# Optimization experiments

Measured on AMD Instinct MI355X. Metric: run time of the kernel, lower is better.

## Reference

```python
import jax, jax.numpy as jnp
import numpy as np

B, T, H, W, C = 2, 6, 16, 16, 256
NUM_HEADS = 8


def light_cone_mask(T, H, W):
    """Boolean mask [N, N] (N = T*H*W): key (t,h,w) is visible to query
    (tq,hq,wq) iff t <= tq and |h-hq|, |w-wq| <= radius(tq, t), where
    radius = int(1 + (max(H,W)-1) * (tq-t) / max(tq,1))  (per the torch loop)."""
    M = max(H, W)
    tq = jnp.arange(T)[:, None]
    tk = jnp.arange(T)[None, :]
    # values are >= 0 on the causal region, so floor == int() truncation
    r = jnp.floor(1.0 + (M - 1) * (tq - tk) / jnp.maximum(tq, 1)).astype(jnp.int32)  # [T,T]
    causal = tk <= tq  # [T,T]
    dh = jnp.abs(jnp.arange(H)[:, None] - jnp.arange(H)[None, :])  # [Hq,Hk]
    dw = jnp.abs(jnp.arange(W)[:, None] - jnp.arange(W)[None, :])  # [Wq,Wk]
    m = (causal[:, None, None, :, None, None]
         & (dh[None, :, None, None, :, None] <= r[:, None, None, :, None, None])
         & (dw[None, None, :, None, None, :] <= r[:, None, None, :, None, None]))
    return m.reshape(T * H * W, T * H * W)


def setup_inputs() -> dict:
    key = jax.random.key(0)
    k1, k2, k3 = jax.random.split(key, 3)
    x = jax.random.normal(k1, (B, T, H, W, C), dtype=jnp.float32)
    Wqkv = jax.random.normal(k2, (C, 3 * C), dtype=jnp.float32) * 0.02
    Wo = jax.random.normal(k3, (C, C), dtype=jnp.float32) * 0.02
    bo = jnp.zeros((C,), dtype=jnp.float32)
    return {"x": x, "Wqkv": Wqkv, "Wo": Wo, "bo": bo}


def reference(x, Wqkv, Wo, bo):
    Bx, Tx, Hx, Wx, Cx = x.shape
    nh = NUM_HEADS
    hd = Cx // nh
    scale = hd ** (-0.5)
    N = Tx * Hx * Wx
    xt = x.reshape(Bx, N, Cx)
    qkv = (xt @ Wqkv).reshape(Bx, N, 3, nh, hd)
    q = qkv[:, :, 0].transpose(0, 2, 1, 3)  # [B, nh, N, hd]
    k = qkv[:, :, 1].transpose(0, 2, 1, 3)
    v = qkv[:, :, 2].transpose(0, 2, 1, 3)
    scores = jnp.einsum("bhqd,bhkd->bhqk", q, k) * scale  # [B, nh, N, N]
    mask = light_cone_mask(Tx, Hx, Wx)  # [N, N]
    neg = jnp.asarray(-1e9, dtype=scores.dtype)
    scores = jnp.where(mask[None, None, :, :], scores, neg)
    attn = jax.nn.softmax(scores, axis=-1)
    out = jnp.einsum("bhqk,bhkd->bhqd", attn, v)  # [B, nh, N, hd]
    out = out.transpose(0, 2, 1, 3).reshape(Bx, N, Cx)
    out = out @ Wo + bo
    return out.reshape(Bx, Tx, Hx, Wx, Cx)
```

## Files before the change

kernel.cpp:

```cpp
#include <hip/hip_runtime.h>
#include <hip/hip_bf16.h>

#define BB   2
#define TT   6
#define HH   16
#define WW   16
#define CC   256
#define NH   8
#define HD   32
#define NN   (TT*HH*WW)
#define BN   (BB*NN)
#define SCALE 0.17677669529663687f

typedef __attribute__((ext_vector_type(8))) short bf16x8;
typedef __attribute__((ext_vector_type(4))) short bf16x4;
typedef __attribute__((ext_vector_type(4))) float f32x4;
typedef __attribute__((ext_vector_type(16))) float f32x16;

static __device__ inline short f2b(float x) {
    __hip_bfloat16 h = __float2bfloat16(x);
    return __builtin_bit_cast(short, h);
}

__global__ __launch_bounds__(256) void gemm1_qkv(const float* __restrict__ x,
                                                 const float* __restrict__ Wqkv,
                                                 short* __restrict__ Qb,
                                                 short* __restrict__ Kb,
                                                 short* __restrict__ VT) {
    const int w = threadIdx.x >> 6, lane = threadIdx.x & 63;
    const int g = lane >> 4, c16 = lane & 15;
    const int ct = blockIdx.x % 12;
    const int rg = blockIdx.x / 12;
    const int n0 = ct * 64;
    const int mw = rg * 64 + w * 16;
    f32x4 acc[4] = {};
    #pragma unroll
    for (int ks = 0; ks < 8; ++ks) {
        const int k0 = ks * 32;
        const float* ap = x + (size_t)(mw + c16) * 256 + k0 + 8 * g;
        const float4 fa = *(const float4*)ap;
        const float4 fb = *(const float4*)(ap + 4);
        short ta[8] = { f2b(fa.x), f2b(fa.y), f2b(fa.z), f2b(fa.w),
                        f2b(fb.x), f2b(fb.y), f2b(fb.z), f2b(fb.w) };
        const bf16x8 a0 = *(bf16x8*)ta;
        #pragma unroll
        for (int ni = 0; ni < 4; ++ni) {
            const float* wp = Wqkv + (size_t)(k0 + 8 * g) * 768 + n0 + ni * 16 + c16;
            short tw[8];
            #pragma unroll
            for (int i = 0; i < 8; ++i) tw[i] = f2b(wp[(size_t)i * 768]);
            const bf16x8 bfr = *(bf16x8*)tw;
            acc[ni] = __builtin_amdgcn_mfma_f32_16x16x32_bf16(a0, bfr, acc[ni], 0, 0, 0);
        }
    }
    const int sec = ct >> 2;
    const int b = mw >= NN;
    const int nbase = mw - b * NN;
    #pragma unroll
    for (int ni = 0; ni < 4; ++ni) {
        const int col = n0 + ni * 16;
        const int h  = (col >> 5) & 7;
        const int d0 = col & 31;
        const int bh = b * 8 + h;
        if (sec == 2) {
            short t4[4];
            #pragma unroll
            for (int r = 0; r < 4; ++r) t4[r] = f2b(acc[ni][r]);
            const int kt  = nbase >> 5;
            const int klo = (nbase & 16) + 4 * g;
            size_t off = ((size_t)((bh * 48 + kt) * 32) + d0 + c16) * 32 + klo;
            *(bf16x4*)(VT + off) = *(bf16x4*)t4;
        } else {
            short* dst = (sec == 0) ? Qb : Kb;
            const float sc = (sec == 0) ? SCALE : 1.f;
            #pragma unroll
            for (int r = 0; r < 4; ++r)
                dst[((size_t)bh * NN + nbase + 4 * g + r) * 32 + d0 + c16] =
                    f2b(acc[ni][r] * sc);
        }
    }
}

__global__ __launch_bounds__(256) void attn_mfma32(const short* __restrict__ Qb,
                                                   const short* __restrict__ Kb,
                                                   const short* __restrict__ VT,
                                                   const float* __restrict__ Wo,
                                                   short* __restrict__ woT,
                                                   short* __restrict__ aob) {
    const int w    = threadIdx.x >> 6;
    const int lane = threadIdx.x & 63;
    const int l31  = lane & 31;
    const int gb   = lane >> 5;
    const int wq   = lane & 15;
    const int qh   = (lane >> 4) & 1;
    const int task = blockIdx.x;
    const int qt = task % 48, bh = task / 48;
    const int tqp = qt >> 4, hq = qt & 15;
    const int tq_a = 2 * tqp, tq_b = tq_a + 1;

    if (blockIdx.x < 32) {
        const int idx = blockIdx.x * 256 + threadIdx.x;
        const int k0 = (idx & 31) * 8;
        const int n  = idx >> 5;
        short t[8];
        #pragma unroll
        for (int j = 0; j < 8; ++j) t[j] = f2b(Wo[(size_t)(k0 + j) * 256 + n]);
        *(bf16x8*)(woT + (size_t)n * 256 + k0) = *(bf16x8*)t;
    }

    __shared__ int desc[64];
    __shared__ float sm_l[4][64];
    __shared__ float sm_acc[4][64][17];

    const int tq_l = qh ? tq_b : tq_a;
    const int qn   = tq_l * 256 + hq * 16 + wq;
    const short* QBH = Qb + (size_t)bh * NN * 32;
    const bf16x8 qf0 = *(const bf16x8*)(QBH + (size_t)qn * 32 + 8 * gb);
    const bf16x8 qf1 = *(const bf16x8*)(QBH + (size_t)qn * 32 + 16 + 8 * gb);

    int dwv[8];
    #pragma unroll
    for (int i = 0; i < 8; ++i) {
        int kl = (i & 3) + 8 * (i >> 2) + 4 * gb;
        int d = kl - wq; dwv[i] = d < 0 ? -d : d;
    }

    const int tqm_a = tq_a ? tq_a : 1;
    int ntiles = 0;
    int cst[6], h20[6], rtav[6], rtbv[6];
    #pragma unroll
    for (int tk = 0; tk < 6; ++tk) {
        int rb = 1 + (15 * (tq_b - tk)) / tq_b;
        int ra = (tk <= tq_a) ? (1 + (15 * (tq_a - tk)) / tqm_a) : -1;
        int lo = hq - rb; lo = lo < 0 ? 0 : lo;
        int hi = hq + rb; hi = hi > 15 ? 15 : hi;
        int c  = (tk <= tq_b) ? ((hi >> 1) - (lo >> 1) + 1) : 0;
        cst[tk] = ntiles; h20[tk] = lo >> 1; rtav[tk] = ra; rtbv[tk] = rb;
        ntiles += c;
    }

    if (w == 0) {
        const int t = lane;
        int dsc = 255;
        if (t < ntiles) {
            int sel = 0;
            #pragma unroll
            for (int tk = 1; tk < 6; ++tk)
                if (tk <= tq_b && t >= cst[tk]) sel = tk;
            const int hk2 = h20[sel] + (t - cst[sel]);
            dsc = ((sel * 256 + hk2 * 32) << 16) | ((rtav[sel] & 255) << 8) | (rtbv[sel] & 255);
        }
        desc[t] = dsc;
    }
    __syncthreads();

    const short* KBH = Kb + (size_t)bh * NN * 32;
    const short* VBH = VT + (size_t)bh * 48 * 32 * 32;

    f32x16 acc, zf16;
    #pragma unroll
    for (int r = 0; r < 16; ++r) { acc[r] = 0.f; zf16[r] = 0.f; }
    float l_run = 0.f;

    int pi = w;
    int dc = 0;
    bf16x8 kf0c = {}, kf1c = {}, vf0c = {}, vf1c = {};
    if (pi < ntiles) {
        dc = desc[pi];
        const int kb = dc >> 16;
        kf0c = *(const bf16x8*)(KBH + (size_t)(kb + l31) * 32 + 8 * gb);
        kf1c = *(const bf16x8*)(KBH + (size_t)(kb + l31) * 32 + 16 + 8 * gb);
        vf0c = *(const bf16x8*)(VBH + (size_t)((kb >> 5) * 32 + l31) * 32 + 8 * gb);
        vf1c = *(const bf16x8*)(VBH + (size_t)((kb >> 5) * 32 + l31) * 32 + 16 + 8 * gb);
    }
    while (pi < ntiles) {
        const int pn = pi + 4;
        const int pc = pn < ntiles ? pn : pi;
        const int dn = desc[pc];
        const int kbn = dn >> 16;
        const bf16x8 kf0n = *(const bf16x8*)(KBH + (size_t)(kbn + l31) * 32 + 8 * gb);
        const bf16x8 kf1n = *(const bf16x8*)(KBH + (size_t)(kbn + l31) * 32 + 16 + 8 * gb);
        const bf16x8 vf0n = *(const bf16x8*)(VBH + (size_t)((kbn >> 5) * 32 + l31) * 32 + 8 * gb);
        const bf16x8 vf1n = *(const bf16x8*)(VBH + (size_t)((kbn >> 5) * 32 + l31) * 32 + 16 + 8 * gb);

        const int rta = (dc << 16) >> 24;
        const int rtb = (dc << 24) >> 24;
        const int rt_l = qh ? rtb : rta;
        const int hk2 = (dc >> 21) & 7;
        const int t0 = 2 * hk2 - hq;
        const int dh0 = t0 < 0 ? -t0 : t0;
        const int t1 = t0 + 1;
        const int dh1 = t1 < 0 ? -t1 : t1;
        const bool A0 = dh0 <= rt_l, A1 = dh1 <= rt_l;
        bool dok[8];
        #pragma unroll
        for (int i = 0; i < 8; ++i) dok[i] = dwv[i] <= rt_l;

        f32x16 s = __builtin_amdgcn_mfma_f32_32x32x16_bf16(kf0c, qf0, zf16, 0, 0, 0);
        s = __builtin_amdgcn_mfma_f32_32x32x16_bf16(kf1c, qf1, s, 0, 0, 0);

        float p[16];
        #pragma unroll
        for (int r = 0; r < 16; ++r) {
            const bool ok = (r < 8 ? A0 : A1) && dok[r & 7];
            p[r] = ok ? __expf(s[r]) : 0.f;
        }
        float ps = (((p[0] + p[1]) + (p[2] + p[3])) + ((p[4] + p[5]) + (p[6] + p[7])))
                 + (((p[8] + p[9]) + (p[10] + p[11])) + ((p[12] + p[13]) + (p[14] + p[15])));
        l_run += ps;

        unsigned u[8];
        #pragma unroll
        for (int j = 0; j < 8; ++j)
            asm("v_cvt_pk_bf16_f32 %0, %1, %2" : "=v"(u[j]) : "v"(p[2 * j]), "v"(p[2 * j + 1]));
        asm volatile("v_permlane32_swap_b32 %0, %1" : "+v"(u[0]), "+v"(u[2]));
        asm volatile("v_permlane32_swap_b32 %0, %1" : "+v"(u[1]), "+v"(u[3]));
        asm volatile("v_permlane32_swap_b32 %0, %1" : "+v"(u[4]), "+v"(u[6]));
        asm volatile("v_permlane32_swap_b32 %0, %1" : "+v"(u[5]), "+v"(u[7]));
        const int4 b1i = { (int)u[0], (int)u[1], (int)u[2], (int)u[3] };
        const int4 b2i = { (int)u[4], (int)u[5], (int)u[6], (int)u[7] };
        const bf16x8 pb1 = __builtin_bit_cast(bf16x8, b1i);
        const bf16x8 pb2 = __builtin_bit_cast(bf16x8, b2i);

        acc = __builtin_amdgcn_mfma_f32_32x32x16_bf16(vf0c, pb1, acc, 0, 0, 0);
        acc = __builtin_amdgcn_mfma_f32_32x32x16_bf16(vf1c, pb2, acc, 0, 0, 0);

        pi = pn; dc = dn;
        kf0c = kf0n; kf1c = kf1n; vf0c = vf0n; vf1c = vf1n;
    }

    sm_l[w][lane] = l_run;
    #pragma unroll
    for (int r = 0; r < 16; ++r) sm_acc[w][lane][r] = acc[r];
    __syncthreads();
    {
        const float lt = (sm_l[0][l31] + sm_l[0][l31 + 32])
                       + (sm_l[1][l31] + sm_l[1][l31 + 32])
                       + (sm_l[2][l31] + sm_l[2][l31 + 32])
                       + (sm_l[3][l31] + sm_l[3][l31 + 32]);
        const float inv = 1.f / lt;
        short* op = aob + ((size_t)(bh >> 3) * NN + qn) * CC + (bh & 7) * 32;
        short t4[4];
        #pragma unroll
        for (int s2 = 0; s2 < 4; ++s2) {
            const int r = 4 * w + s2;
            const float a = sm_acc[0][lane][r] + sm_acc[1][lane][r]
                          + sm_acc[2][lane][r] + sm_acc[3][lane][r];
            t4[s2] = f2b(a * inv);
        }
        *(bf16x4*)(op + 8 * w + 4 * gb) = *(bf16x4*)t4;
    }
}

__global__ __launch_bounds__(256) void gemm2_out(const short* __restrict__ aob,
                                                 const short* __restrict__ woT,
                                                 const float* __restrict__ bias,
                                                 float* __restrict__ out) {
    const int w = threadIdx.x >> 6, lane = threadIdx.x & 63;
    const int g = lane >> 4, c16 = lane & 15;
    const int n0 = (blockIdx.x & 3) * 64;
    const int mw = (blockIdx.x >> 2) * 64 + w * 16;
    f32x4 acc[4] = {};
    #pragma unroll
    for (int ks = 0; ks < 8; ++ks) {
        const int k0 = ks * 32;
        const bf16x8 a0 = *(const bf16x8*)(aob + (size_t)(mw + c16) * 256 + k0 + g * 8);
        #pragma unroll
        for (int ni = 0; ni < 4; ++ni) {
            const bf16x8 bfr = *(const bf16x8*)(woT + (size_t)(n0 + ni * 16 + c16) * 256 + k0 + g * 8);
            acc[ni] = __builtin_amdgcn_mfma_f32_16x16x32_bf16(a0, bfr, acc[ni], 0, 0, 0);
        }
    }
    #pragma unroll
    for (int ni = 0; ni < 4; ++ni) {
        const int col = n0 + ni * 16 + c16;
        const float bv = bias[col];
        #pragma unroll
        for (int r = 0; r < 4; ++r)
            out[(size_t)(mw + 4 * g + r) * 256 + col] = acc[ni][r] + bv;
    }
}

extern "C" void kernel_launch(void* const* d_in, const int* in_sizes, int n_in,
                              void* d_out, int out_size, void* d_ws, size_t ws_size,
                              hipStream_t stream) {
    const float* x    = (const float*)d_in[0];
    const float* Wqkv = (const float*)d_in[1];
    const float* Wo   = (const float*)d_in[2];
    const float* bo   = (const float*)d_in[3];
    float* out = (float*)d_out;

    short* Qb  = (short*)d_ws;
    short* Kb  = Qb  + 786432;
    short* VT  = Kb  + 786432;
    short* aob = VT  + 786432;
    short* woT = aob + 786432;

    gemm1_qkv<<<576, 256, 0, stream>>>(x, Wqkv, Qb, Kb, VT);
    attn_mfma32<<<768, 256, 0, stream>>>(Qb, Kb, VT, Wo, woT, aob);
    gemm2_out<<<192, 256, 0, stream>>>(aob, woT, bo, out);
}
```

Before: 36.67 us.

## Stage Wqkv in LDS, fold log2e into Q scale, compute tile descriptors inline

The QKV GEMM now loads and converts its 64-column Wqkv slice once per block into swizzled shared memory, so the four waves share it instead of each doing strided global loads and conversions. Q is prescaled by log2(e), which lets the attention kernel use a raw v_exp_f32 (exp2) in place of __expf. The shared-memory descriptor table and its block barrier are replaced by a per-lane select chain that computes each tile's key base and radii in registers. The GEMM gains 32KB of LDS and a barrier, which may lower occupancy. The attention kernel does more ALU work per tile in exchange for dropping the LDS reads and the sync.

After: 35.19 us, median of 2. 1.04x faster.

```diff
diff --git a/kernel.cpp b/kernel.cpp
--- a/kernel.cpp
+++ b/kernel.cpp
@@ -11,6 +11,7 @@
 #define NN   (TT*HH*WW)
 #define BN   (BB*NN)
 #define SCALE 0.17677669529663687f
+#define SCALE_L2E (0.17677669529663687f * 1.4426950408889634f)
 
 typedef __attribute__((ext_vector_type(8))) short bf16x8;
 typedef __attribute__((ext_vector_type(4))) short bf16x4;
@@ -20,6 +21,12 @@
 static __device__ inline short f2b(float x) {
     __hip_bfloat16 h = __float2bfloat16(x);
     return __builtin_bit_cast(short, h);
+}
+
+static __device__ inline float exp2_raw(float x) {
+    float r;
+    asm("v_exp_f32 %0, %1" : "=v"(r) : "v"(x));
+    return r;
 }
 
 __global__ __launch_bounds__(256) void gemm1_qkv(const float* __restrict__ x,
@@ -27,12 +34,33 @@
                                                  short* __restrict__ Qb,
                                                  short* __restrict__ Kb,
                                                  short* __restrict__ VT) {
-    const int w = threadIdx.x >> 6, lane = threadIdx.x & 63;
+    const int tid = threadIdx.x;
+    const int w = tid >> 6, lane = tid & 63;
     const int g = lane >> 4, c16 = lane & 15;
     const int ct = blockIdx.x % 12;
     const int rg = blockIdx.x / 12;
     const int n0 = ct * 64;
     const int mw = rg * 64 + w * 16;
+
+    __shared__ short wlds[64 * 256];
+    char* const wbase = (char*)wlds;
+
+    {
+        const int n_l = tid & 63;
+        const int kc  = tid >> 6;
+        const int sw  = (n_l & 7) << 4;
+        #pragma unroll
+        for (int it = 0; it < 8; ++it) {
+            const int k0s = it * 32 + kc * 8;
+            const float* wp = Wqkv + (size_t)k0s * 768 + n0 + n_l;
+            short t8[8];
+            #pragma unroll
+            for (int i = 0; i < 8; ++i) t8[i] = f2b(wp[(size_t)i * 768]);
+            *(bf16x8*)(wbase + n_l * 512 + ((k0s * 2) ^ sw)) = *(bf16x8*)t8;
+        }
+    }
+    __syncthreads();
+
     f32x4 acc[4] = {};
     #pragma unroll
     for (int ks = 0; ks < 8; ++ks) {
@@ -45,11 +73,9 @@
         const bf16x8 a0 = *(bf16x8*)ta;
         #pragma unroll
         for (int ni = 0; ni < 4; ++ni) {
-            const float* wp = Wqkv + (size_t)(k0 + 8 * g) * 768 + n0 + ni * 16 + c16;
-            short tw[8];
-            #pragma unroll
-            for (int i = 0; i < 8; ++i) tw[i] = f2b(wp[(size_t)i * 768]);
-            const bf16x8 bfr = *(bf16x8*)tw;
+            const int n_l2 = ni * 16 + c16;
+            const bf16x8 bfr = *(const bf16x8*)(wbase + n_l2 * 512 +
+                                  ((ks * 64 + g * 16) ^ ((n_l2 & 7) << 4)));
             acc[ni] = __builtin_amdgcn_mfma_f32_16x16x32_bf16(a0, bfr, acc[ni], 0, 0, 0);
         }
     }
@@ -72,7 +98,7 @@
             *(bf16x4*)(VT + off) = *(bf16x4*)t4;
         } else {
             short* dst = (sec == 0) ? Qb : Kb;
-            const float sc = (sec == 0) ? SCALE : 1.f;
+            const float sc = (sec == 0) ? SCALE_L2E : 1.f;
             #pragma unroll
             for (int r = 0; r < 4; ++r)
                 dst[((size_t)bh * NN + nbase + 4 * g + r) * 32 + d0 + c16] =
@@ -108,7 +134,6 @@
         *(bf16x8*)(woT + (size_t)n * 256 + k0) = *(bf16x8*)t;
     }
 
-    __shared__ int desc[64];
     __shared__ float sm_l[4][64];
     __shared__ float sm_acc[4][64][17];
 
@@ -139,20 +164,20 @@
         ntiles += c;
     }
 
-    if (w == 0) {
-        const int t = lane;
-        int dsc = 255;
-        if (t < ntiles) {
-            int sel = 0;
-            #pragma unroll
-            for (int tk = 1; tk < 6; ++tk)
-                if (tk <= tq_b && t >= cst[tk]) sel = tk;
-            const int hk2 = h20[sel] + (t - cst[sel]);
-            dsc = ((sel * 256 + hk2 * 32) << 16) | ((rtav[sel] & 255) << 8) | (rtbv[sel] & 255);
-        }
-        desc[t] = dsc;
-    }
-    __syncthreads();
+    auto tiledesc = [&](int t, int& kb, int& ra, int& rb) {
+        int sc_ = cst[0], sh_ = h20[0], sa_ = rtav[0], sb_ = rtbv[0], st_ = 0;
+        #pragma unroll
+        for (int tk = 1; tk < 6; ++tk) {
+            const bool sel = (tk <= tq_b) && (t >= cst[tk]);
+            sc_ = sel ? cst[tk]  : sc_;
+            sh_ = sel ? h20[tk]  : sh_;
+            sa_ = sel ? rtav[tk] : sa_;
+            sb_ = sel ? rtbv[tk] : sb_;
+            st_ = sel ? tk       : st_;
+        }
+        kb = st_ * 256 + (sh_ + (t - sc_)) * 32;
+        ra = sa_; rb = sb_;
+    };
 
     const short* KBH = Kb + (size_t)bh * NN * 32;
     const short* VBH = VT + (size_t)bh * 48 * 32 * 32;
@@ -163,11 +188,10 @@
     float l_run = 0.f;
 
     int pi = w;
-    int dc = 0;
+    int kb = 0, ra = -1, rb = -1;
     bf16x8 kf0c = {}, kf1c = {}, vf0c = {}, vf1c = {};
     if (pi < ntiles) {
-        dc = desc[pi];
-        const int kb = dc >> 16;
+        tiledesc(pi, kb, ra, rb);
         kf0c = *(const bf16x8*)(KBH + (size_t)(kb + l31) * 32 + 8 * gb);
         kf1c = *(const bf16x8*)(KBH + (size_t)(kb + l31) * 32 + 16 + 8 * gb);
         vf0c = *(const bf16x8*)(VBH + (size_t)((kb >> 5) * 32 + l31) * 32 + 8 * gb);
@@ -175,18 +199,15 @@
     }
     while (pi < ntiles) {
         const int pn = pi + 4;
-        const int pc = pn < ntiles ? pn : pi;
-        const int dn = desc[pc];
-        const int kbn = dn >> 16;
+        int kbn, ran, rbn;
+        tiledesc(pn < ntiles ? pn : pi, kbn, ran, rbn);
         const bf16x8 kf0n = *(const bf16x8*)(KBH + (size_t)(kbn + l31) * 32 + 8 * gb);
         const bf16x8 kf1n = *(const bf16x8*)(KBH + (size_t)(kbn + l31) * 32 + 16 + 8 * gb);
         const bf16x8 vf0n = *(const bf16x8*)(VBH + (size_t)((kbn >> 5) * 32 + l31) * 32 + 8 * gb);
         const bf16x8 vf1n = *(const bf16x8*)(VBH + (size_t)((kbn >> 5) * 32 + l31) * 32 + 16 + 8 * gb);
 
-        const int rta = (dc << 16) >> 24;
-        const int rtb = (dc << 24) >> 24;
-        const int rt_l = qh ? rtb : rta;
-        const int hk2 = (dc >> 21) & 7;
+        const int rt_l = qh ? rb : ra;
+        const int hk2 = (kb >> 5) & 7;
         const int t0 = 2 * hk2 - hq;
         const int dh0 = t0 < 0 ? -t0 : t0;
         const int t1 = t0 + 1;
@@ -203,7 +224,7 @@
         #pragma unroll
         for (int r = 0; r < 16; ++r) {
             const bool ok = (r < 8 ? A0 : A1) && dok[r & 7];
-            p[r] = ok ? __expf(s[r]) : 0.f;
+            p[r] = ok ? exp2_raw(s[r]) : 0.f;
         }
         float ps = (((p[0] + p[1]) + (p[2] + p[3])) + ((p[4] + p[5]) + (p[6] + p[7])))
                  + (((p[8] + p[9]) + (p[10] + p[11])) + ((p[12] + p[13]) + (p[14] + p[15])));
@@ -225,7 +246,7 @@
         acc = __builtin_amdgcn_mfma_f32_32x32x16_bf16(vf0c, pb1, acc, 0, 0, 0);
         acc = __builtin_amdgcn_mfma_f32_32x32x16_bf16(vf1c, pb2, acc, 0, 0, 0);
 
-        pi = pn; dc = dn;
+        pi = pn; kb = kbn; ra = ran; rb = rbn;
         kf0c = kf0n; kf1c = kf1n; vf0c = vf0n; vf1c = vf1n;
     }
 
```
